# Kernel tuning notes

Hardware: AMD Instinct MI355X
Metric: run time of the kernel (lower is better)

## Reference

```python
import jax, jax.numpy as jnp
import numpy as np

N_NODES = 10000
N_EDGES = 320000
HIDDEN = 16      # hidden_state_size
MSG = 64         # message_size
EDGE_FEAT = 32


def setup_inputs() -> dict:
    key = jax.random.key(0)
    ks = jax.random.split(key, 8)
    node_features = jax.random.normal(ks[0], (N_NODES, HIDDEN), dtype=jnp.float32)
    edge_features = jax.random.normal(ks[1], (N_EDGES, EDGE_FEAT), dtype=jnp.float32)
    edge_sources = jax.random.randint(ks[2], (N_EDGES,), 0, N_NODES, dtype=jnp.int32)
    edge_targets = jax.random.randint(ks[3], (N_EDGES,), 0, N_NODES, dtype=jnp.int32)
    hidden = jax.random.normal(ks[4], (N_NODES, HIDDEN), dtype=jnp.float32)
    initial = jax.random.normal(ks[5], (N_NODES, HIDDEN), dtype=jnp.float32)
    # Dense(edge_feat -> MSG*HIDDEN), glorot-ish scale
    W = jax.random.normal(ks[6], (EDGE_FEAT, MSG * HIDDEN), dtype=jnp.float32) / np.float32(np.sqrt(EDGE_FEAT))
    b = jnp.zeros((MSG * HIDDEN,), dtype=jnp.float32)
    return {
        "node_features": node_features,
        "edge_features": edge_features,
        "edge_sources": edge_sources,
        "edge_targets": edge_targets,
        "hidden": hidden,
        "initial": initial,
        "W": W,
        "b": b,
    }


def reference(node_features, edge_features, edge_sources, edge_targets, hidden, initial, W, b):
    # Per edge: edge_mat = Dense(edge_feat) reshaped (MSG, HIDDEN);
    # message = edge_mat @ hidden[source]; aggregate = sum over incoming edges per target node.
    num_nodes = node_features.shape[0]
    edge_mat = (edge_features @ W + b).reshape(-1, MSG, HIDDEN)  # [E, M, H]
    neigh = hidden[edge_sources]                                  # [E, H] gather
    messages = jnp.einsum("emh,eh->em", edge_mat, neigh)         # [E, M] batched matvec
    out = jax.ops.segment_sum(messages, edge_targets, num_segments=num_nodes)  # [N, M]
    return out
```

## Files before the change

### kernel.cpp

```cpp
#include <hip/hip_runtime.h>
#include <hip/hip_bf16.h>

#define N_NODES 10000
#define N_EDGES 320000
#define HIDDEN 16
#define MSG 64
#define EDGE_FEAT 32
#define KSTEPS 17
#define EPB 128

typedef __attribute__((ext_vector_type(2))) _Float16 f16x2;
typedef __attribute__((ext_vector_type(4))) _Float16 f16x4;
typedef __attribute__((ext_vector_type(8))) _Float16 f16x8;
typedef __attribute__((ext_vector_type(4))) float    f32x4;

union H8 { f16x8 v; f16x2 p[4]; f16x4 q[2]; };

__global__ void zero_prep(const float* __restrict__ W, const float* __restrict__ bias,
                          ushort* __restrict__ WrB, int* __restrict__ cnt,
                          float4* __restrict__ out4, int n4) {
    if (blockIdx.x < KSTEPS) {
        const int ks   = blockIdx.x;
        const int nt   = threadIdx.x >> 6;
        const int lane = threadIdx.x & 63;
        const int g    = lane >> 4;
        const int n    = nt * 16 + (lane & 15);
        ushort* dst = WrB + (((size_t)ks * 4 + nt) * 64 + lane) * 8;
        #pragma unroll
        for (int i = 0; i < 8; ++i) {
            const int k = ks * 32 + g * 8 + i;
            float v;
            if (k < 512)      v = W[(size_t)(k >> 4) * 1024 + n * 16 + (k & 15)];
            else if (k < 528) v = bias[n * 16 + (k - 512)];
            else              v = 0.0f;
            const _Float16 hv = (_Float16)v;
            dst[i] = *reinterpret_cast<const ushort*>(&hv);
        }
    } else if (blockIdx.x < KSTEPS + 40) {
        const int idx = (blockIdx.x - KSTEPS) * 256 + threadIdx.x;
        if (idx < N_NODES) cnt[idx] = 0;
    } else {
        const int i = (blockIdx.x - KSTEPS - 40) * 256 + threadIdx.x;
        if (i < n4) out4[i] = make_float4(0.f, 0.f, 0.f, 0.f);
    }
}

__global__ __launch_bounds__(256) void rank_kernel(const int* __restrict__ tgt,
                                                   int* __restrict__ cnt,
                                                   int* __restrict__ rank) {
    const int e = blockIdx.x * 256 + threadIdx.x;
    if (e < N_EDGES) rank[e] = atomicAdd(&cnt[tgt[e]], 1);
}

__global__ __launch_bounds__(1024) void scan_kernel(const int* __restrict__ cnt,
                                                    int* __restrict__ starts) {
    __shared__ int wsum[16];
    __shared__ int wbase[16];
    const int tid  = threadIdx.x;
    const int lane = tid & 63;
    const int wv   = tid >> 6;
    int c[10];
    int s = 0;
    #pragma unroll
    for (int j = 0; j < 10; ++j) {
        const int idx = tid * 10 + j;
        c[j] = (idx < N_NODES) ? cnt[idx] : 0;
        s += c[j];
    }
    int v = s;
    #pragma unroll
    for (int d = 1; d < 64; d <<= 1) {
        const int u = __shfl_up(v, d);
        if (lane >= d) v += u;
    }
    if (lane == 63) wsum[wv] = v;
    __syncthreads();
    if (tid < 16) {
        const int w = wsum[tid];
        int iv = w;
        #pragma unroll
        for (int d = 1; d < 16; d <<= 1) {
            const int u = __shfl_up(iv, d);
            if (tid >= d) iv += u;
        }
        wbase[tid] = iv - w;
    }
    __syncthreads();
    int running = wbase[wv] + (v - s);
    #pragma unroll
    for (int j = 0; j < 10; ++j) {
        const int idx = tid * 10 + j;
        if (idx < N_NODES) starts[idx] = running;
        running += c[j];
    }
    if (tid == 1023) starts[N_NODES] = N_EDGES;
}

__global__ __launch_bounds__(256) void build_desc(
    const int* __restrict__ tgt, const int* __restrict__ rank,
    const int* __restrict__ starts, const int* __restrict__ src,
    int4* __restrict__ edesc) {
    const int e = blockIdx.x * 256 + threadIdx.x;
    if (e < N_EDGES) {
        const int t = tgt[e];
        edesc[starts[t] + rank[e]] = make_int4(e, src[e], t, 0);
    }
}

__global__ __launch_bounds__(256, 5) void fused_msg(
    const int4*   __restrict__ edesc,
    const float*  __restrict__ ef,
    const float*  __restrict__ hidden,
    const ushort* __restrict__ WrB,
    float*        __restrict__ out)
{
    __shared__ _Float16 ef_h[EPB][36];
    __shared__ _Float16 nb_h[EPB][16];
    __shared__ int      tgt_s[EPB];
    __shared__ _Float16 msg_h[EPB][68];

    const int tid = threadIdx.x;
    const int s0  = blockIdx.x * EPB;

    {
        const int sl = tid >> 1;
        const int hf = tid & 1;
        const int4 d = edesc[s0 + sl];
        const int e  = d.x;
        const int sn = d.y;

        const float4* ep = (const float4*)(ef + (size_t)e * EDGE_FEAT + hf * 16);
        const float4 v0 = ep[0], v1 = ep[1], v2 = ep[2], v3 = ep[3];
        _Float16* dst = &ef_h[sl][hf * 16];
        *(f16x4*)(dst + 0)  = f16x4{(_Float16)v0.x, (_Float16)v0.y, (_Float16)v0.z, (_Float16)v0.w};
        *(f16x4*)(dst + 4)  = f16x4{(_Float16)v1.x, (_Float16)v1.y, (_Float16)v1.z, (_Float16)v1.w};
        *(f16x4*)(dst + 8)  = f16x4{(_Float16)v2.x, (_Float16)v2.y, (_Float16)v2.z, (_Float16)v2.w};
        *(f16x4*)(dst + 12) = f16x4{(_Float16)v3.x, (_Float16)v3.y, (_Float16)v3.z, (_Float16)v3.w};

        const float4* hp = (const float4*)(hidden + (size_t)sn * HIDDEN + hf * 8);
        const float4 h0 = hp[0], h1 = hp[1];
        *(f16x8*)&nb_h[sl][hf * 8] =
            f16x8{(_Float16)h0.x, (_Float16)h0.y, (_Float16)h0.z, (_Float16)h0.w,
                  (_Float16)h1.x, (_Float16)h1.y, (_Float16)h1.z, (_Float16)h1.w};

        if (hf) {
            ef_h[sl][32] = (_Float16)1.0f;
            ef_h[sl][33] = (_Float16)0.0f;
            ef_h[sl][34] = (_Float16)0.0f;
            ef_h[sl][35] = (_Float16)0.0f;
        } else {
            tgt_s[sl] = d.z;
        }
    }
    __syncthreads();

    const int wave = tid >> 6;
    const int lane = tid & 63;
    const int er   = lane & 15;
    const int g    = lane >> 4;
    const int eA   = wave * 32 + er;
    const int eB   = eA + 16;
    const int hoff = (g & 1) * 8;
    const int fg   = g >> 1;

    H8 nbA, nbB;
    nbA.v = *(const f16x8*)&nb_h[eA][hoff];
    nbB.v = *(const f16x8*)&nb_h[eB][hoff];

    f32x4 aA0 = {0.f,0.f,0.f,0.f}, aA1 = aA0, aA2 = aA0, aA3 = aA0;
    f32x4 aB0 = aA0, aB1 = aA0, aB2 = aA0, aB3 = aA0;
    const f16x8* Bp = (const f16x8*)WrB;

    #pragma unroll
    for (int ks = 0; ks < KSTEPS; ++ks) {
        const f16x8 b0 = Bp[(ks * 4 + 0) * 64 + lane];
        const f16x8 b1 = Bp[(ks * 4 + 1) * 64 + lane];
        const f16x8 b2 = Bp[(ks * 4 + 2) * 64 + lane];
        const f16x8 b3 = Bp[(ks * 4 + 3) * 64 + lane];

        const _Float16 a_A = ef_h[eA][2 * ks + fg];
        const _Float16 a_B = ef_h[eB][2 * ks + fg];
        const f16x2 avA = {a_A, a_A};
        const f16x2 avB = {a_B, a_B};
        H8 afA, afB;
        #pragma unroll
        for (int q = 0; q < 4; ++q) {
            afA.p[q] = avA * nbA.p[q];
            afB.p[q] = avB * nbB.p[q];
        }
        aA0 = __builtin_amdgcn_mfma_f32_16x16x32_f16(afA.v, b0, aA0, 0, 0, 0);
        aA1 = __builtin_amdgcn_mfma_f32_16x16x32_f16(afA.v, b1, aA1, 0, 0, 0);
        aA2 = __builtin_amdgcn_mfma_f32_16x16x32_f16(afA.v, b2, aA2, 0, 0, 0);
        aA3 = __builtin_amdgcn_mfma_f32_16x16x32_f16(afA.v, b3, aA3, 0, 0, 0);
        aB0 = __builtin_amdgcn_mfma_f32_16x16x32_f16(afB.v, b0, aB0, 0, 0, 0);
        aB1 = __builtin_amdgcn_mfma_f32_16x16x32_f16(afB.v, b1, aB1, 0, 0, 0);
        aB2 = __builtin_amdgcn_mfma_f32_16x16x32_f16(afB.v, b2, aB2, 0, 0, 0);
        aB3 = __builtin_amdgcn_mfma_f32_16x16x32_f16(afB.v, b3, aB3, 0, 0, 0);
    }

    #pragma unroll
    for (int r = 0; r < 4; ++r) {
        const int rowA = wave * 32 + g * 4 + r;
        msg_h[rowA][ 0 + er] = (_Float16)aA0[r];
        msg_h[rowA][16 + er] = (_Float16)aA1[r];
        msg_h[rowA][32 + er] = (_Float16)aA2[r];
        msg_h[rowA][48 + er] = (_Float16)aA3[r];
        const int rowB = rowA + 16;
        msg_h[rowB][ 0 + er] = (_Float16)aB0[r];
        msg_h[rowB][16 + er] = (_Float16)aB1[r];
        msg_h[rowB][32 + er] = (_Float16)aB2[r];
        msg_h[rowB][48 + er] = (_Float16)aB3[r];
    }
    __syncthreads();

    const int c = tid & 63;
    const int rbase = (tid >> 6) * 32;
    float run = (float)msg_h[rbase][c];
    int   cur = tgt_s[rbase];
    #pragma unroll
    for (int r = 1; r < 32; ++r) {
        const int   tg = tgt_s[rbase + r];
        const float m  = (float)msg_h[rbase + r][c];
        if (tg != cur) {
            atomicAdd(out + (size_t)cur * MSG + c, run);
            cur = tg;
            run = m;
        } else {
            run += m;
        }
    }
    atomicAdd(out + (size_t)cur * MSG + c, run);
}

__global__ __launch_bounds__(256) void zero_out(float* __restrict__ p, int n4) {
    const int i = blockIdx.x * 256 + threadIdx.x;
    if (i < n4) ((float4*)p)[i] = make_float4(0.f, 0.f, 0.f, 0.f);
}

__global__ __launch_bounds__(256, 4) void msg_mfma(
    const float* __restrict__ ef, const int* __restrict__ src,
    const int* __restrict__ tgt, const float* __restrict__ hidden,
    const ushort* __restrict__ WrB, float* __restrict__ out)
{
    __shared__ float ef_s[64][36];
    __shared__ float neigh_s[64][20];
    __shared__ int   tgt_s[64];
    const int tid = threadIdx.x;
    const int e0  = blockIdx.x * 64;
    {
        const int e = tid >> 2, h4 = (tid & 3) * 4;
        const int s = src[e0 + e];
        *(float4*)&neigh_s[e][h4] = *(const float4*)(hidden + (size_t)s * HIDDEN + h4);
    }
    {
        const int e = tid >> 2, f8 = (tid & 3) * 8;
        const float* p = ef + (size_t)(e0 + e) * EDGE_FEAT + f8;
        *(float4*)&ef_s[e][f8]     = *(const float4*)(p);
        *(float4*)&ef_s[e][f8 + 4] = *(const float4*)(p + 4);
    }
    if (tid < 64) { ef_s[tid][32] = 1.0f; ef_s[tid][33] = 0.0f; tgt_s[tid] = tgt[e0 + tid]; }
    __syncthreads();
    const int wave = tid >> 6, lane = tid & 63;
    const int er = lane & 15, g = lane >> 4;
    const int e_loc = wave * 16 + er;
    const int h0 = (g & 1) * 8, fg = g >> 1;
    float nb[8];
    #pragma unroll
    for (int j = 0; j < 8; ++j) nb[j] = neigh_s[e_loc][h0 + j];
    f32x4 acc0 = {0.f,0.f,0.f,0.f}, acc1 = acc0, acc2 = acc0, acc3 = acc0;
    const f16x8* Bp = (const f16x8*)WrB;
    #pragma unroll
    for (int ks = 0; ks < KSTEPS; ++ks) {
        const float a = ef_s[e_loc][2 * ks + fg];
        f16x8 af;
        #pragma unroll
        for (int j = 0; j < 8; ++j) af[j] = (_Float16)(a * nb[j]);
        const f16x8 b0 = Bp[(ks * 4 + 0) * 64 + lane];
        const f16x8 b1 = Bp[(ks * 4 + 1) * 64 + lane];
        const f16x8 b2 = Bp[(ks * 4 + 2) * 64 + lane];
        const f16x8 b3 = Bp[(ks * 4 + 3) * 64 + lane];
        acc0 = __builtin_amdgcn_mfma_f32_16x16x32_f16(af, b0, acc0, 0, 0, 0);
        acc1 = __builtin_amdgcn_mfma_f32_16x16x32_f16(af, b1, acc1, 0, 0, 0);
        acc2 = __builtin_amdgcn_mfma_f32_16x16x32_f16(af, b2, acc2, 0, 0, 0);
        acc3 = __builtin_amdgcn_mfma_f32_16x16x32_f16(af, b3, acc3, 0, 0, 0);
    }
    #pragma unroll
    for (int r = 0; r < 4; ++r) {
        const int t = tgt_s[wave * 16 + g * 4 + r];
        float* op = out + (size_t)t * MSG;
        atomicAdd(op +      er, acc0[r]);
        atomicAdd(op + 16 + er, acc1[r]);
        atomicAdd(op + 32 + er, acc2[r]);
        atomicAdd(op + 48 + er, acc3[r]);
    }
}

extern "C" void kernel_launch(void* const* d_in, const int* in_sizes, int n_in,
                              void* d_out, int out_size, void* d_ws, size_t ws_size,
                              hipStream_t stream) {
    const float* ef     = (const float*)d_in[1];
    const int*   src    = (const int*)d_in[2];
    const int*   tgt    = (const int*)d_in[3];
    const float* hidden = (const float*)d_in[4];
    const float* W      = (const float*)d_in[6];
    const float* bias   = (const float*)d_in[7];
    float* out = (float*)d_out;
    char*  ws  = (char*)d_ws;

    const size_t o_wrb    = 0;
    const size_t o_starts = 69632;
    const size_t o_cnt    = 109648;
    const size_t o_rank   = 149648;
    const size_t o_desc   = 1429648;
    const size_t need     = o_desc + (size_t)N_EDGES * 16;

    ushort* WrB = (ushort*)(ws + o_wrb);
    const int n4 = out_size / 4;

    if (ws_size >= need) {
        int*  starts = (int*)(ws + o_starts);
        int*  cnt    = (int*)(ws + o_cnt);
        int*  rank   = (int*)(ws + o_rank);
        int4* edesc  = (int4*)(ws + o_desc);

        const int zb_cnt = 40;
        const int zb_out = (n4 + 255) / 256;
        zero_prep<<<KSTEPS + zb_cnt + zb_out, 256, 0, stream>>>(W, bias, WrB, cnt,
                                                                (float4*)out, n4);
        rank_kernel<<<(N_EDGES + 255) / 256, 256, 0, stream>>>(tgt, cnt, rank);
        scan_kernel<<<1, 1024, 0, stream>>>(cnt, starts);
        build_desc<<<(N_EDGES + 255) / 256, 256, 0, stream>>>(tgt, rank, starts, src, edesc);
        fused_msg<<<N_EDGES / EPB, 256, 0, stream>>>(edesc, ef, hidden, WrB, out);
    } else {
        zero_prep<<<KSTEPS, 256, 0, stream>>>(W, bias, WrB, nullptr, nullptr, 0);
        zero_out<<<(n4 + 255) / 256, 256, 0, stream>>>(out, n4);
        msg_mfma<<<N_EDGES / 64, 256, 0, stream>>>(ef, src, tgt, hidden, WrB, out);
    }
}
```

Measured before the change: 76.64 us.

## Split MFMA work by output column tile per wave instead of by edge rows

Each wave now owns one 16-column slice of the message output across all 128 edges in the block, rather than all 64 columns for 32 edges. A wave loads one B fragment per k-step instead of four, cutting global/L2 reads of the weight matrix fourfold. In exchange every wave must rebuild the A operands (edge feature times neighbor hidden) for all 8 row tiles, which adds VALU work and LDS reads of ef_h and nb_h.

```diff
diff --git a/kernel.cpp b/kernel.cpp
--- a/kernel.cpp
+++ b/kernel.cpp
@@ -154,62 +154,44 @@
     }
     __syncthreads();
 
-    const int wave = tid >> 6;
+    const int nt   = tid >> 6;
     const int lane = tid & 63;
     const int er   = lane & 15;
     const int g    = lane >> 4;
-    const int eA   = wave * 32 + er;
-    const int eB   = eA + 16;
     const int hoff = (g & 1) * 8;
     const int fg   = g >> 1;
 
-    H8 nbA, nbB;
-    nbA.v = *(const f16x8*)&nb_h[eA][hoff];
-    nbB.v = *(const f16x8*)&nb_h[eB][hoff];
-
-    f32x4 aA0 = {0.f,0.f,0.f,0.f}, aA1 = aA0, aA2 = aA0, aA3 = aA0;
-    f32x4 aB0 = aA0, aB1 = aA0, aB2 = aA0, aB3 = aA0;
+    H8 nb[8];
+    #pragma unroll
+    for (int rt = 0; rt < 8; ++rt)
+        nb[rt].v = *(const f16x8*)&nb_h[rt * 16 + er][hoff];
+
+    f32x4 acc[8];
+    #pragma unroll
+    for (int rt = 0; rt < 8; ++rt) acc[rt] = f32x4{0.f, 0.f, 0.f, 0.f};
+
     const f16x8* Bp = (const f16x8*)WrB;
 
     #pragma unroll
     for (int ks = 0; ks < KSTEPS; ++ks) {
-        const f16x8 b0 = Bp[(ks * 4 + 0) * 64 + lane];
-        const f16x8 b1 = Bp[(ks * 4 + 1) * 64 + lane];
-        const f16x8 b2 = Bp[(ks * 4 + 2) * 64 + lane];
-        const f16x8 b3 = Bp[(ks * 4 + 3) * 64 + lane];
-
-        const _Float16 a_A = ef_h[eA][2 * ks + fg];
-        const _Float16 a_B = ef_h[eB][2 * ks + fg];
-        const f16x2 avA = {a_A, a_A};
-        const f16x2 avB = {a_B, a_B};
-        H8 afA, afB;
-        #pragma unroll
-        for (int q = 0; q < 4; ++q) {
-            afA.p[q] = avA * nbA.p[q];
-            afB.p[q] = avB * nbB.p[q];
-        }
-        aA0 = __builtin_amdgcn_mfma_f32_16x16x32_f16(afA.v, b0, aA0, 0, 0, 0);
-        aA1 = __builtin_amdgcn_mfma_f32_16x16x32_f16(afA.v, b1, aA1, 0, 0, 0);
-        aA2 = __builtin_amdgcn_mfma_f32_16x16x32_f16(afA.v, b2, aA2, 0, 0, 0);
-        aA3 = __builtin_amdgcn_mfma_f32_16x16x32_f16(afA.v, b3, aA3, 0, 0, 0);
-        aB0 = __builtin_amdgcn_mfma_f32_16x16x32_f16(afB.v, b0, aB0, 0, 0, 0);
-        aB1 = __builtin_amdgcn_mfma_f32_16x16x32_f16(afB.v, b1, aB1, 0, 0, 0);
-        aB2 = __builtin_amdgcn_mfma_f32_16x16x32_f16(afB.v, b2, aB2, 0, 0, 0);
-        aB3 = __builtin_amdgcn_mfma_f32_16x16x32_f16(afB.v, b3, aB3, 0, 0, 0);
-    }
-
-    #pragma unroll
-    for (int r = 0; r < 4; ++r) {
-        const int rowA = wave * 32 + g * 4 + r;
-        msg_h[rowA][ 0 + er] = (_Float16)aA0[r];
-        msg_h[rowA][16 + er] = (_Float16)aA1[r];
-        msg_h[rowA][32 + er] = (_Float16)aA2[r];
-        msg_h[rowA][48 + er] = (_Float16)aA3[r];
-        const int rowB = rowA + 16;
-        msg_h[rowB][ 0 + er] = (_Float16)aB0[r];
-        msg_h[rowB][16 + er] = (_Float16)aB1[r];
-        msg_h[rowB][32 + er] = (_Float16)aB2[r];
-        msg_h[rowB][48 + er] = (_Float16)aB3[r];
+        const f16x8 b = Bp[(ks * 4 + nt) * 64 + lane];
+        #pragma unroll
+        for (int rt = 0; rt < 8; ++rt) {
+            const _Float16 a = ef_h[rt * 16 + er][2 * ks + fg];
+            const f16x2 av = {a, a};
+            H8 af;
+            #pragma unroll
+            for (int q = 0; q < 4; ++q) af.p[q] = av * nb[rt].p[q];
+            acc[rt] = __builtin_amdgcn_mfma_f32_16x16x32_f16(af.v, b, acc[rt], 0, 0, 0);
+        }
+    }
+
+    #pragma unroll
+    for (int rt = 0; rt < 8; ++rt) {
+        #pragma unroll
+        for (int r = 0; r < 4; ++r) {
+            msg_h[rt * 16 + g * 4 + r][nt * 16 + er] = (_Float16)acc[rt][r];
+        }
     }
     __syncthreads();
 
```

Result: no change. 77.76 us (+1.5%).
